# Optimization experiments

Measured on AMD Instinct MI355X. Metric: run time of the kernel, lower is better.

## Reference

```python
import jax, jax.numpy as jnp
import numpy as np

B, N, H, E = 2, 1024, 128, 32

def setup_inputs() -> dict:
    key = jax.random.key(0)
    ks = jax.random.split(key, 8)
    node_features = jax.random.normal(ks[0], (B, N, H), dtype=jnp.float32)
    # sparse-ish binary static adjacency mask
    adjacency_matrix = (jax.random.uniform(ks[1], (N, N)) < 0.05).astype(jnp.float32)
    s = 1.0 / np.sqrt(H)
    Wt = jax.random.uniform(ks[2], (H, H), minval=-s, maxval=s, dtype=jnp.float32)
    bt = jax.random.uniform(ks[3], (H,), minval=-s, maxval=s, dtype=jnp.float32)
    s1 = 1.0 / np.sqrt(2 * H)
    W1 = jax.random.uniform(ks[4], (E, 2 * H), minval=-s1, maxval=s1, dtype=jnp.float32)
    b1 = jax.random.uniform(ks[5], (E,), minval=-s1, maxval=s1, dtype=jnp.float32)
    s2 = 1.0 / np.sqrt(E)
    W2 = jax.random.uniform(ks[6], (1, E), minval=-s2, maxval=s2, dtype=jnp.float32)
    b2 = jax.random.uniform(ks[7], (1,), minval=-s2, maxval=s2, dtype=jnp.float32)
    return {"node_features": node_features, "adjacency_matrix": adjacency_matrix,
            "Wt": Wt, "bt": bt, "W1": W1, "b1": b1, "W2": W2, "b2": b2}

def reference(node_features, adjacency_matrix, Wt, bt, W1, b1, W2, b2):
    # node transform: [B,N,H]
    t = jnp.einsum('bnh,oh->bno', node_features, Wt) + bt
    # split first edge-MLP layer: W1 @ [h_i, h_j] = W1i @ h_i + W1j @ h_j
    W1i, W1j = W1[:, :t.shape[-1]], W1[:, t.shape[-1]:]
    hi = jnp.einsum('bnh,eh->bne', t, W1i)  # [B,N,E]
    hj = jnp.einsum('bnh,eh->bne', t, W1j)  # [B,N,E]
    h = jax.nn.relu(hi[:, :, None, :] + hj[:, None, :, :] + b1)  # [B,N,N,E]
    edge_weights = jnp.einsum('bnme,e->bnm', h, W2[0]) + b2[0]   # [B,N,N]
    dynamic_adj = jax.nn.sigmoid(edge_weights) * adjacency_matrix[None]
    return dynamic_adj
```

## Files before the change

### kernel.cpp

```cpp
#include <hip/hip_runtime.h>
#include <math.h>

#define NN 1024
#define PADW 132


__global__ __launch_bounds__(256) void gall_kernel(
    const float* __restrict__ nf, const float* __restrict__ Wt,
    const float* __restrict__ bt, const float* __restrict__ W1,
    const float* __restrict__ b1, float* __restrict__ gall)
{
    __shared__ float s_w[64 * PADW];
    __shared__ float s_nf[4 * 128];
    __shared__ float s_t[4 * PADW];
    __shared__ float s_bt[128];
    __shared__ float s_b1[32];

    const int tid = threadIdx.x;
    const int nb  = blockIdx.x * 4;

    for (int idx = tid; idx < 4 * 128; idx += 256)
        s_nf[idx] = nf[nb * 128 + idx];
    if (tid < 128) s_bt[tid] = bt[tid];
    else if (tid < 160) s_b1[tid - 128] = b1[tid - 128];

    const int n_own = tid >> 6;
    const int o_own = tid & 63;

    #pragma unroll
    for (int hf = 0; hf < 2; ++hf) {
        __syncthreads();
        for (int idx = tid; idx < 2048; idx += 256) {
            const int o = idx >> 5, hc = idx & 31;
            *reinterpret_cast<float4*>(s_w + o * PADW + 4 * hc) =
                *reinterpret_cast<const float4*>(Wt + (hf * 64 + o) * 128 + 4 * hc);
        }
        __syncthreads();

        const float* wrow = s_w + o_own * PADW;
        const float* nrow = s_nf + n_own * 128;
        float4 A = {0.f, 0.f, 0.f, 0.f};
        #pragma unroll 8
        for (int hc = 0; hc < 32; ++hc) {
            const float4 w = *reinterpret_cast<const float4*>(wrow + 4 * hc);
            const float4 x = *reinterpret_cast<const float4*>(nrow + 4 * hc);
            A.x = fmaf(w.x, x.x, A.x);
            A.y = fmaf(w.y, x.y, A.y);
            A.z = fmaf(w.z, x.z, A.z);
            A.w = fmaf(w.w, x.w, A.w);
        }
        const int o = hf * 64 + o_own;
        s_t[n_own * PADW + o] = (A.x + A.y) + (A.z + A.w) + s_bt[o];
    }

    __syncthreads();
    for (int idx = tid; idx < 2048; idx += 256) {
        const int ep = idx >> 5, oc = idx & 31;
        const int e = ep & 31, half = ep >> 5;
        *reinterpret_cast<float4*>(s_w + ep * PADW + 4 * oc) =
            *reinterpret_cast<const float4*>(W1 + e * 256 + half * 128 + 4 * oc);
    }
    __syncthreads();
    {
        const int ep = tid & 63;
        const float* wrow = s_w + ep * PADW;
        const float* trow = s_t + n_own * PADW;
        float4 A = {0.f, 0.f, 0.f, 0.f};
        #pragma unroll 8
        for (int oc = 0; oc < 32; ++oc) {
            const float4 w = *reinterpret_cast<const float4*>(wrow + 4 * oc);
            const float4 x = *reinterpret_cast<const float4*>(trow + 4 * oc);
            A.x = fmaf(w.x, x.x, A.x);
            A.y = fmaf(w.y, x.y, A.y);
            A.z = fmaf(w.z, x.z, A.z);
            A.w = fmaf(w.w, x.w, A.w);
        }
        float g = (A.x + A.y) + (A.z + A.w);
        if ((ep >> 5) == 0) g += s_b1[ep & 31];
        gall[(nb + n_own) * 64 + ep] = g;
    }
}

__global__ __launch_bounds__(256) void edge_kernel(
    const float* __restrict__ adj, const float* __restrict__ gall,
    const float* __restrict__ W2, const float* __restrict__ b2,
    float* __restrict__ out)
{
    const int n   = blockIdx.x;
    const int tid = threadIdx.x;

    __shared__ float s_u[2][32];
    __shared__ float s_w2[32];
    __shared__ unsigned s_cnt;
    __shared__ unsigned short s_ent[2048];
    __shared__ float s_res[2048];

    const int m0 = tid * 4;
    const float4 a4 = *reinterpret_cast<const float4*>(adj + n * NN + m0);

    if (tid < 32)       s_u[0][tid]       = gall[n * 64 + tid];
    else if (tid < 64)  s_u[1][tid & 31]  = gall[(NN + n) * 64 + (tid & 31)];
    else if (tid < 96)  s_w2[tid & 31]    = W2[tid & 31];
    if (tid == 0) s_cnt = 0;
    __syncthreads();

    const float* ap = &a4.x;
    int eidx[8];
    #pragma unroll
    for (int b = 0; b < 2; ++b) {
        #pragma unroll
        for (int cc = 0; cc < 4; ++cc) {
            const int slot = b * 4 + cc;
            eidx[slot] = -1;
            if (ap[cc] != 0.f) {
                const unsigned w = atomicAdd(&s_cnt, 1u);
                s_ent[w] = (unsigned short)((b << 10) | (m0 + cc));
                eidx[slot] = (int)w;
            }
        }
    }
    __syncthreads();
    const unsigned cnt = s_cnt;
    const float b2v = b2[0];

    for (unsigned w = tid; w < cnt; w += 256) {
        const unsigned ent = s_ent[w];
        const int bb = ent >> 10, m = ent & 1023;
        const float* gj = gall + (bb * NN + m) * 64 + 32;
        const float* uu = s_u[bb];
        float ew = b2v;
        #pragma unroll
        for (int j = 0; j < 8; ++j) {
            const float4 gv = *reinterpret_cast<const float4*>(gj + 4 * j);
            ew = fmaf(fmaxf(uu[4 * j + 0] + gv.x, 0.f), s_w2[4 * j + 0], ew);
            ew = fmaf(fmaxf(uu[4 * j + 1] + gv.y, 0.f), s_w2[4 * j + 1], ew);
            ew = fmaf(fmaxf(uu[4 * j + 2] + gv.z, 0.f), s_w2[4 * j + 2], ew);
            ew = fmaf(fmaxf(uu[4 * j + 3] + gv.w, 0.f), s_w2[4 * j + 3], ew);
        }
        s_res[w] = 1.f / (1.f + __expf(-ew));
    }
    __syncthreads();

    #pragma unroll
    for (int b = 0; b < 2; ++b) {
        float4 r4;
        float* rp = &r4.x;
        #pragma unroll
        for (int cc = 0; cc < 4; ++cc) {
            const int slot = b * 4 + cc;
            rp[cc] = (eidx[slot] >= 0) ? ap[cc] * s_res[eidx[slot]] : 0.f;
        }
        *reinterpret_cast<float4*>(out + (size_t)(b * NN + n) * NN + m0) = r4;
    }
}

extern "C" void kernel_launch(void* const* d_in, const int* in_sizes, int n_in,
                              void* d_out, int out_size, void* d_ws, size_t ws_size,
                              hipStream_t stream)
{
    const float* nf  = (const float*)d_in[0];
    const float* adj = (const float*)d_in[1];
    const float* Wt  = (const float*)d_in[2];
    const float* bt  = (const float*)d_in[3];
    const float* W1  = (const float*)d_in[4];
    const float* b1  = (const float*)d_in[5];
    const float* W2  = (const float*)d_in[6];
    const float* b2  = (const float*)d_in[7];
    float* out  = (float*)d_out;
    float* gall = (float*)d_ws;

    hipLaunchKernelGGL(gall_kernel, dim3(512), dim3(256), 0, stream,
                       nf, Wt, bt, W1, b1, gall);
    hipLaunchKernelGGL(edge_kernel, dim3(NN), dim3(256), 0, stream,
                       adj, gall, W2, b2, out);
}
```

Measured before the change: 19.54 us.

## Precompute adjacency bitmask in first kernel and use prefix-sum compaction in edge kernel

The first kernel now also reads the adjacency matrix and packs each row into a 32-word bitmask stored in workspace. The edge kernel reads this mask instead of the dense float row, and builds its compact list of nonzero columns with a popcount prefix sum instead of shared-memory atomics. Both batches share one entry list. This removes the dense adjacency read from the edge kernel and the atomic contention, but adds extra adjacency reads and syncs to the first kernel. The output also drops the multiply by the adjacency value, which assumes the mask holds only 0/1 values.

```diff
diff --git a/kernel.cpp b/kernel.cpp
--- a/kernel.cpp
+++ b/kernel.cpp
@@ -4,25 +4,55 @@
 #define NN 1024
 #define PADW 132
 
+
+__device__ __forceinline__ float hsum4(float4 a) {
+    return (a.x + a.y) + (a.z + a.w);
+}
 
 __global__ __launch_bounds__(256) void gall_kernel(
     const float* __restrict__ nf, const float* __restrict__ Wt,
     const float* __restrict__ bt, const float* __restrict__ W1,
-    const float* __restrict__ b1, float* __restrict__ gall)
+    const float* __restrict__ b1, const float* __restrict__ adj,
+    float* __restrict__ gall, unsigned* __restrict__ mask)
 {
     __shared__ float s_w[64 * PADW];
     __shared__ float s_nf[4 * 128];
     __shared__ float s_t[4 * PADW];
     __shared__ float s_bt[128];
     __shared__ float s_b1[32];
+    __shared__ unsigned s_nib[256];
 
     const int tid = threadIdx.x;
-    const int nb  = blockIdx.x * 4;
+    const int bid = blockIdx.x;
+    const int nb  = bid * 4;
+
+    const float4 ar0 = *reinterpret_cast<const float4*>(adj + (2 * bid + 0) * NN + tid * 4);
+    const float4 ar1 = *reinterpret_cast<const float4*>(adj + (2 * bid + 1) * NN + tid * 4);
 
     for (int idx = tid; idx < 4 * 128; idx += 256)
         s_nf[idx] = nf[nb * 128 + idx];
     if (tid < 128) s_bt[tid] = bt[tid];
     else if (tid < 160) s_b1[tid - 128] = b1[tid - 128];
+
+    s_nib[tid] = (unsigned)(ar0.x != 0.f) | ((unsigned)(ar0.y != 0.f) << 1) |
+                 ((unsigned)(ar0.z != 0.f) << 2) | ((unsigned)(ar0.w != 0.f) << 3);
+    __syncthreads();
+    if (tid < 32) {
+        unsigned d = 0;
+        #pragma unroll
+        for (int k = 0; k < 8; ++k) d |= s_nib[8 * tid + k] << (4 * k);
+        mask[(2 * bid + 0) * 32 + tid] = d;
+    }
+    __syncthreads();
+    s_nib[tid] = (unsigned)(ar1.x != 0.f) | ((unsigned)(ar1.y != 0.f) << 1) |
+                 ((unsigned)(ar1.z != 0.f) << 2) | ((unsigned)(ar1.w != 0.f) << 3);
+    __syncthreads();
+    if (tid < 32) {
+        unsigned d = 0;
+        #pragma unroll
+        for (int k = 0; k < 8; ++k) d |= s_nib[8 * tid + k] << (4 * k);
+        mask[(2 * bid + 1) * 32 + tid] = d;
+    }
 
     const int n_own = tid >> 6;
     const int o_own = tid & 63;
@@ -50,7 +80,7 @@
             A.w = fmaf(w.w, x.w, A.w);
         }
         const int o = hf * 64 + o_own;
-        s_t[n_own * PADW + o] = (A.x + A.y) + (A.z + A.w) + s_bt[o];
+        s_t[n_own * PADW + o] = hsum4(A) + s_bt[o];
     }
 
     __syncthreads();
@@ -75,14 +105,14 @@
             A.z = fmaf(w.z, x.z, A.z);
             A.w = fmaf(w.w, x.w, A.w);
         }
-        float g = (A.x + A.y) + (A.z + A.w);
+        float g = hsum4(A);
         if ((ep >> 5) == 0) g += s_b1[ep & 31];
         gall[(nb + n_own) * 64 + ep] = g;
     }
 }
 
 __global__ __launch_bounds__(256) void edge_kernel(
-    const float* __restrict__ adj, const float* __restrict__ gall,
+    const float* __restrict__ gall, const unsigned* __restrict__ mask,
     const float* __restrict__ W2, const float* __restrict__ b2,
     float* __restrict__ out)
 {
@@ -91,41 +121,46 @@
 
     __shared__ float s_u[2][32];
     __shared__ float s_w2[32];
-    __shared__ unsigned s_cnt;
-    __shared__ unsigned short s_ent[2048];
-    __shared__ float s_res[2048];
+    __shared__ unsigned s_mask[32];
+    __shared__ unsigned s_pre[33];
+    __shared__ unsigned short s_ent[NN];
+    __shared__ float s_res[2 * NN];
+
+    if (tid < 32)       s_u[0][tid]      = gall[n * 64 + tid];
+    else if (tid < 64)  s_u[1][tid & 31] = gall[(NN + n) * 64 + (tid & 31)];
+    else if (tid < 96)  s_w2[tid & 31]   = W2[tid & 31];
+    else if (tid < 128) s_mask[tid & 31] = mask[n * 32 + (tid & 31)];
+    __syncthreads();
+
+    if (tid < 32) {
+        unsigned sum = 0;
+        for (int d = 0; d < tid; ++d) sum += __popc(s_mask[d]);
+        s_pre[tid] = sum;
+        if (tid == 31) s_pre[32] = sum + __popc(s_mask[31]);
+    }
+    __syncthreads();
 
     const int m0 = tid * 4;
-    const float4 a4 = *reinterpret_cast<const float4*>(adj + n * NN + m0);
-
-    if (tid < 32)       s_u[0][tid]       = gall[n * 64 + tid];
-    else if (tid < 64)  s_u[1][tid & 31]  = gall[(NN + n) * 64 + (tid & 31)];
-    else if (tid < 96)  s_w2[tid & 31]    = W2[tid & 31];
-    if (tid == 0) s_cnt = 0;
-    __syncthreads();
-
-    const float* ap = &a4.x;
-    int eidx[8];
+    const unsigned dw = s_mask[tid >> 3];
+    int eidx[4];
     #pragma unroll
-    for (int b = 0; b < 2; ++b) {
-        #pragma unroll
-        for (int cc = 0; cc < 4; ++cc) {
-            const int slot = b * 4 + cc;
-            eidx[slot] = -1;
-            if (ap[cc] != 0.f) {
-                const unsigned w = atomicAdd(&s_cnt, 1u);
-                s_ent[w] = (unsigned short)((b << 10) | (m0 + cc));
-                eidx[slot] = (int)w;
-            }
-        }
-    }
-    __syncthreads();
-    const unsigned cnt = s_cnt;
+    for (int cc = 0; cc < 4; ++cc) {
+        const int bitpos = 4 * (tid & 7) + cc;
+        if ((dw >> bitpos) & 1u) {
+            const int p = (int)s_pre[tid >> 3] + __popc(dw & ((1u << bitpos) - 1u));
+            s_ent[p] = (unsigned short)(m0 + cc);
+            eidx[cc] = p;
+        } else {
+            eidx[cc] = -1;
+        }
+    }
+    __syncthreads();
+    const int cnt = (int)s_pre[32];
     const float b2v = b2[0];
 
-    for (unsigned w = tid; w < cnt; w += 256) {
-        const unsigned ent = s_ent[w];
-        const int bb = ent >> 10, m = ent & 1023;
+    for (int w = tid; w < 2 * cnt; w += 256) {
+        const int bb = (w >= cnt);
+        const int m  = s_ent[w - bb * cnt];
         const float* gj = gall + (bb * NN + m) * 64 + 32;
         const float* uu = s_u[bb];
         float ew = b2v;
@@ -141,17 +176,21 @@
     }
     __syncthreads();
 
+    float4 r0, r1;
+    float* rp0 = &r0.x;
+    float* rp1 = &r1.x;
     #pragma unroll
-    for (int b = 0; b < 2; ++b) {
-        float4 r4;
-        float* rp = &r4.x;
-        #pragma unroll
-        for (int cc = 0; cc < 4; ++cc) {
-            const int slot = b * 4 + cc;
-            rp[cc] = (eidx[slot] >= 0) ? ap[cc] * s_res[eidx[slot]] : 0.f;
-        }
-        *reinterpret_cast<float4*>(out + (size_t)(b * NN + n) * NN + m0) = r4;
-    }
+    for (int cc = 0; cc < 4; ++cc) {
+        if (eidx[cc] >= 0) {
+            rp0[cc] = s_res[eidx[cc]];
+            rp1[cc] = s_res[cnt + eidx[cc]];
+        } else {
+            rp0[cc] = 0.f;
+            rp1[cc] = 0.f;
+        }
+    }
+    *reinterpret_cast<float4*>(out + (size_t)n * NN + m0) = r0;
+    *reinterpret_cast<float4*>(out + (size_t)(NN + n) * NN + m0) = r1;
 }
 
 extern "C" void kernel_launch(void* const* d_in, const int* in_sizes, int n_in,
@@ -168,9 +207,10 @@
     const float* b2  = (const float*)d_in[7];
     float* out  = (float*)d_out;
     float* gall = (float*)d_ws;
+    unsigned* mask = (unsigned*)(gall + 2048 * 64);
 
     hipLaunchKernelGGL(gall_kernel, dim3(512), dim3(256), 0, stream,
-                       nf, Wt, bt, W1, b1, gall);
+                       nf, Wt, bt, W1, b1, adj, gall, mask);
     hipLaunchKernelGGL(edge_kernel, dim3(NN), dim3(256), 0, stream,
-                       adj, gall, W2, b2, out);
-}
+                       gall, mask, W2, b2, out);
+}
```

New measurement: 20.64 us. 1.06x slower.
